# Kernel optimization log

Measured on AMD Instinct MI355X. Metric: run time of the kernel, lower is better.

The kernel has to match this reference:

```python
import jax, jax.numpy as jnp
import numpy as np

N, Q, CC = 8, 300, 92          # batch, queries, logit channels (91 classes + 1 objectness)
CF, HF, WF = 2048, 42, 42      # backbone feature map
M, TOPK = 20, 5                # GT boxes per image, pseudo-unknown top-k
NUM_CLASSES = 91
L_CLS, L_IOU, L_L1 = 2.0, 2.0, 5.0
NEG = -1e11


def cxcywh_to_xyxy(bx):
    cx, cy, bw, bh = bx[..., 0], bx[..., 1], bx[..., 2], bx[..., 3]
    return jnp.stack([cx - bw / 2, cy - bh / 2, cx + bw / 2, cy + bh / 2], -1)


def setup_inputs() -> dict:
    key = jax.random.key(0)
    ks = jax.random.split(key, 6)
    h = w = 1333
    img_features = jax.random.normal(ks[0], (N, CF, HF, WF), jnp.float32)
    pred_logits = jax.random.normal(ks[1], (N, Q, CC), jnp.float32)
    pred_boxes = jax.random.uniform(ks[2], (N, Q, 4), jnp.float32, 0.05, 0.95)
    tgt_labels = jax.random.randint(ks[3], (N, M), 0, NUM_CLASSES - 1).astype(jnp.int32)
    u = jax.random.uniform(ks[4], (N, M, 4), jnp.float32)
    # GT boxes in pixel cxcywh (bbox_normalize divides by image size)
    tgt_boxes = jnp.stack([u[..., 0] * w, u[..., 1] * h,
                           u[..., 2] * 0.3 * w + 2.0, u[..., 3] * 0.3 * h + 2.0], -1)
    perm = jax.vmap(lambda k: jax.random.permutation(k, Q))(jax.random.split(ks[5], N))
    query_idx = perm[:, :M].astype(jnp.int32)          # unique matched query per target
    tgt_idx = jnp.tile(jnp.arange(M, dtype=jnp.int32), (N, 1))
    return dict(img_features=img_features, pred_logits=pred_logits, pred_boxes=pred_boxes,
                tgt_labels=tgt_labels, tgt_boxes=tgt_boxes, query_idx=query_idx,
                tgt_idx=tgt_idx, h=h, w=w)


def _loss(img_features, pred_logits, pred_boxes, tgt_boxes, tgt_labels, query_idx, tgt_idx, h, w):
    b = jnp.arange(N)[:, None]
    scale = jnp.array([w, h, w, h], jnp.float32)
    out_prob = jnp.concatenate([jax.nn.softmax(pred_logits[..., :-1], -1),
                                jax.nn.sigmoid(pred_logits[..., -1:])], -1)  # [N,Q,92]
    matched_mask = jnp.zeros((N, Q), bool).at[b, query_idx].set(True)

    # --- per-query crop-mean pooling: bilinear upsample once + summed-area table ---
    mean_feat = jnp.mean(img_features, 1)                                  # [N,HF,WF]
    up = jax.vmap(lambda f: jax.image.resize(f, (h, w), 'bilinear'))(mean_feat)  # [N,h,w]
    sat = jnp.pad(jnp.cumsum(jnp.cumsum(up, 1), 2), ((0, 0), (1, 0), (1, 0)))    # [N,h+1,w+1]
    bb = cxcywh_to_xyxy(pred_boxes) * scale                                # pixel xyxy
    x1 = jnp.clip(bb[..., 0].astype(jnp.int32), 0, w)
    y1 = jnp.clip(bb[..., 1].astype(jnp.int32), 0, h)
    x2 = jnp.clip(bb[..., 2].astype(jnp.int32), 0, w)
    y2 = jnp.clip(bb[..., 3].astype(jnp.int32), 0, h)
    cnt = jnp.maximum(y2 - y1, 0) * jnp.maximum(x2 - x1, 0)
    x2e, y2e = jnp.maximum(x2, x1), jnp.maximum(y2, y1)
    boxsum = sat[b, y2e, x2e] - sat[b, y1, x2e] - sat[b, y2e, x1] + sat[b, y1, x1]
    means = jnp.where(cnt > 0, boxsum / jnp.maximum(cnt, 1), NEG)          # empty crop -> -1e11 (nan case)
    means = jnp.where(matched_mask, NEG, means)                            # matched queries excluded
    _, topk_idx = jax.lax.top_k(means, TOPK)                               # [N,TOPK]
    topk_mask = jnp.zeros((N, Q), bool).at[b, topk_idx].set(True)

    # --- matched terms ---
    tgt_cls = tgt_labels[b, tgt_idx]                                       # [N,M]
    tgt_bb = tgt_boxes[b, tgt_idx] / scale                                 # bbox_normalize
    q_cls = out_prob[b, query_idx, :NUM_CLASSES]                           # probs; CE re-applies log_softmax (faithful)
    q_obj = out_prob[b, query_idx, -1]
    q_bb = pred_boxes[b, query_idx]
    logp = jax.nn.log_softmax(q_cls, -1)
    ce_matched = -jnp.mean(jnp.take_along_axis(logp, tgt_cls[..., None].astype(jnp.int32), -1)[..., 0], 1)
    bce_matched = -jnp.mean(jnp.maximum(jnp.log(q_obj), -100.0), 1)
    l1 = jnp.sqrt(jnp.sum((q_bb - tgt_bb) ** 2, (1, 2)))                   # torch.dist (Frobenius)
    a, t = cxcywh_to_xyxy(q_bb), cxcywh_to_xyxy(tgt_bb)
    ix1 = jnp.maximum(a[..., 0], t[..., 0]); iy1 = jnp.maximum(a[..., 1], t[..., 1])
    ix2 = jnp.minimum(a[..., 2], t[..., 2]); iy2 = jnp.minimum(a[..., 3], t[..., 3])
    inter = jnp.clip(ix2 - ix1, 0.0) * jnp.clip(iy2 - iy1, 0.0)
    area = lambda z: (z[..., 2] - z[..., 0]) * (z[..., 3] - z[..., 1])
    iou = inter / (area(a) + area(t) - inter + 1e-9)
    iou_loss = jnp.sum(1.0 - iou, 1)

    # --- pseudo-unknown terms ---
    pk_cls = out_prob[b, topk_idx, :NUM_CLASSES]
    ce_pseudo = -jnp.mean(jax.nn.log_softmax(pk_cls, -1)[..., NUM_CLASSES - 1], 1)
    pk_obj = out_prob[b, topk_idx, -1]
    bce_topk = -jnp.mean(jnp.maximum(jnp.log(pk_obj), -100.0), 1)
    rest = (~matched_mask) & (~topk_mask)                                  # setdiff(other, topk)
    neglog1m = -jnp.maximum(jnp.log1p(-out_prob[..., -1]), -100.0)
    bce_rest = jnp.sum(jnp.where(rest, neglog1m, 0.0), 1) / jnp.maximum(jnp.sum(rest, 1), 1)

    cls_loss = jnp.sum(ce_matched + ce_pseudo)
    obj_loss = jnp.sum(bce_matched + bce_rest + bce_topk)
    return (cls_loss * L_CLS + obj_loss * L_CLS
            + jnp.sum(iou_loss) * L_IOU + jnp.sum(l1) * L_L1)


def reference(img_features, pred_logits, pred_boxes, tgt_labels, tgt_boxes, query_idx, tgt_idx, h, w):
    return _loss(img_features, pred_logits, pred_boxes, tgt_boxes, tgt_labels, query_idx, tgt_idx, h, w)
```

## Files before the change

kernel.cpp:

```cpp
#include <hip/hip_runtime.h>
#include <math.h>

#define NB 8
#define QN 300
#define CCH 92
#define NCLS 91
#define CFCH 2048
#define HFD 42
#define MT 20
#define TOPK5 5
#define DIM 1333
#define DIMF 1333.0f
#define PIX (HFD*HFD)
#define PIX4 (PIX/4)
#define CHUNKS 32
#define CPC (CFCH/CHUNKS)
#define NEGV -100000000000.0f

#define PART_BLOCKS (NB*CHUNKS*2)
#define CUM_TOTAL   (2*(DIM+1)*HFD)
#define CUM_BLOCKS  ((CUM_TOTAL + 255)/256)
#define STAT_BLOCKS ((NB*QN)/4)
#define BM_BLOCKS   ((NB*QN)/4)

__device__ __forceinline__ float bilin_w(int i, int j, float s) {
    float sf = ((float)i + 0.5f) * s - 0.5f;
    if (sf <= 0.f)                return (j == 0) ? 1.f : 0.f;
    if (sf >= (float)(HFD - 1))   return (j == HFD - 1) ? 1.f : 0.f;
    int j0 = (int)sf;
    float fr = sf - (float)j0;
    if (j == j0)     return 1.f - fr;
    if (j == j0 + 1) return fr;
    return 0.f;
}

__device__ __forceinline__ float wave_sum(float v) {
    for (int off = 32; off; off >>= 1) v += __shfl_down(v, off);
    return v;
}

__global__ __launch_bounds__(256) void stage_a(
        const float4* __restrict__ img, float4* __restrict__ part,
        float* __restrict__ CX, float* __restrict__ CY,
        const float* __restrict__ logits, const float* __restrict__ boxes,
        const int* __restrict__ query_idx, const int* __restrict__ tgt_idx,
        const int* __restrict__ tgt_labels, const float* __restrict__ tgt_boxes,
        float* __restrict__ ls2a, float* __restrict__ p90a,
        float* __restrict__ ptga, float* __restrict__ nobja,
        float* __restrict__ n1ma, float* __restrict__ l1a,
        float* __restrict__ ioua, float* __restrict__ out) {
    int blk = blockIdx.x;
    if (blk == 0 && threadIdx.x == 0) out[0] = 0.f;
    if (blk < PART_BLOCKS) {
        int tile = blk & 1;
        int chunk = (blk >> 1) & (CHUNKS - 1);
        int b = blk >> 6;
        int f = tile * 256 + threadIdx.x;
        if (f >= PIX4) return;
        const float4* p = img + (size_t)(b * CFCH + chunk * CPC) * PIX4 + f;
        float x = 0.f, y = 0.f, z = 0.f, w = 0.f;
#pragma unroll 8
        for (int k = 0; k < CPC; ++k) {
            float4 v = p[(size_t)k * PIX4];
            x += v.x; y += v.y; z += v.z; w += v.w;
        }
        float4 o; o.x = x; o.y = y; o.z = z; o.w = w;
        part[(size_t)(blk >> 1) * PIX4 + f] = o;
    } else if (blk < PART_BLOCKS + CUM_BLOCKS) {
        int idx = (blk - PART_BLOCKS) * 256 + threadIdx.x;
        const int total = (DIM + 1) * HFD;
        int t = idx / total;
        if (t >= 2) return;
        int rem = idx - t * total;
        int X = rem / HFD;
        int j = rem - X * HFD;
        const float s = (float)HFD / DIMF;
        int i0 = max(0, (int)floorf(((float)j - 0.5f) / s - 0.5f) - 2);
        int i1 = min(DIM, (int)ceilf(((float)j + 1.5f) / s - 0.5f) + 2);
        int hi = min(X, i1);
        float acc = 0.f;
        for (int i = i0; i < hi; ++i) acc += bilin_w(i, j, s);
        float* C = t ? CY : CX;
        C[X * HFD + j] = acc;
    } else {
        int gw = (blk - PART_BLOCKS - CUM_BLOCKS) * 4 + (threadIdx.x >> 6);
        int lane = threadIdx.x & 63;
        int b = gw / QN, q = gw - b * QN;
        int mpos = -1;
#pragma unroll
        for (int m = 0; m < MT; ++m) if (query_idx[b * MT + m] == q) mpos = m;
        const float* L = logits + (size_t)gw * CCH;
        float c0 = L[lane];
        float e1 = (lane < CCH - 64) ? L[lane + 64] : 0.f;
        bool has_c1 = (lane < NCLS - 64);
        float mx = fmaxf(c0, has_c1 ? e1 : -3.4e38f);
        for (int off = 32; off; off >>= 1) mx = fmaxf(mx, __shfl_xor(mx, off));
        float se = expf(c0 - mx) + (has_c1 ? expf(e1 - mx) : 0.f);
        for (int off = 32; off; off >>= 1) se += __shfl_xor(se, off);
        float inv = 1.f / se;
        float s2 = expf(expf(c0 - mx) * inv) + (has_c1 ? expf(expf(e1 - mx) * inv) : 0.f);
        for (int off = 32; off; off >>= 1) s2 += __shfl_xor(s2, off);
        float ls2 = logf(s2);
        float l90  = __shfl(e1, 26);
        float lobj = __shfl(e1, 27);
        float p90 = expf(l90 - mx) * inv;
        float sg = 1.f / (1.f + expf(-lobj));
        float nobj = -fmaxf(logf(sg), -100.f);
        float n1m  = -fmaxf(log1pf(-sg), -100.f);

        float ptg = 0.f, l1 = 0.f, iouc = 0.f;
        if (mpos >= 0) {
            const float* bx = boxes + (size_t)gw * 4;
            float cx = bx[0], cy = bx[1], bw = bx[2], bh = bx[3];
            int ti = tgt_idx[b * MT + mpos];
            int tc = tgt_labels[b * MT + ti];
            ptg = expf(L[tc] - mx) * inv;
            const float* tb = tgt_boxes + (size_t)(b * MT + ti) * 4;
            float t0 = tb[0] / DIMF, t1 = tb[1] / DIMF, t2 = tb[2] / DIMF, t3 = tb[3] / DIMF;
            float d0 = cx - t0, d1 = cy - t1, d2 = bw - t2, d3 = bh - t3;
            l1 = d0 * d0 + d1 * d1 + d2 * d2 + d3 * d3;
            float ax1 = cx - bw * 0.5f, ay1 = cy - bh * 0.5f;
            float ax2 = cx + bw * 0.5f, ay2 = cy + bh * 0.5f;
            float tx1 = t0 - t2 * 0.5f, ty1 = t1 - t3 * 0.5f;
            float tx2 = t0 + t2 * 0.5f, ty2 = t1 + t3 * 0.5f;
            float ix1 = fmaxf(ax1, tx1), iy1 = fmaxf(ay1, ty1);
            float ix2 = fminf(ax2, tx2), iy2 = fminf(ay2, ty2);
            float inter = fmaxf(ix2 - ix1, 0.f) * fmaxf(iy2 - iy1, 0.f);
            float aa = (ax2 - ax1) * (ay2 - ay1), at = (tx2 - tx1) * (ty2 - ty1);
            float iou = inter / (aa + at - inter + 1e-9f);
            iouc = 1.f - iou;
        }
        if (lane == 0) {
            ls2a[gw] = ls2; p90a[gw] = p90; ptga[gw] = ptg;
            nobja[gw] = nobj; n1ma[gw] = n1m; l1a[gw] = l1; ioua[gw] = iouc;
        }
    }
}

__global__ __launch_bounds__(256) void chan_reduce(const float* __restrict__ part,
                                                   float* __restrict__ mf) {
    int idx = blockIdx.x * 256 + threadIdx.x;
    if (idx >= NB * PIX) return;
    int b = idx / PIX, pix = idx - b * PIX;
    const float* pp = part + (size_t)b * CHUNKS * PIX + pix;
    float acc = 0.f;
#pragma unroll 8
    for (int c = 0; c < CHUNKS; ++c) acc += pp[(size_t)c * PIX];
    mf[idx] = acc * (1.0f / (float)CFCH);
}

__global__ __launch_bounds__(256) void box_means(
        const float* __restrict__ mf, const float* __restrict__ boxes,
        const int* __restrict__ query_idx,
        const float* __restrict__ CX, const float* __restrict__ CY,
        float* __restrict__ means) {
    int tid = threadIdx.x;
    int gw = (blockIdx.x * 256 + tid) >> 6;
    int lane = tid & 63, wid = tid >> 6;
    int b = gw / QN, q = gw - b * QN;

    __shared__ float s_mf[PIX];
    __shared__ float s_d[4][84];
    for (int i = tid; i < PIX; i += 256) s_mf[i] = mf[b * PIX + i];
    __syncthreads();

    int mpos = -1;
#pragma unroll
    for (int m = 0; m < MT; ++m) if (query_idx[b * MT + m] == q) mpos = m;

    const float* bx = boxes + (size_t)gw * 4;
    float cx = bx[0], cy = bx[1], bw = bx[2], bh = bx[3];
    int x1 = min(max((int)((cx - bw * 0.5f) * DIMF), 0), DIM);
    int y1 = min(max((int)((cy - bh * 0.5f) * DIMF), 0), DIM);
    int x2 = min(max((int)((cx + bw * 0.5f) * DIMF), 0), DIM);
    int y2 = min(max((int)((cy + bh * 0.5f) * DIMF), 0), DIM);
    int x2e = max(x2, x1), y2e = max(y2, y1);
    int cnt = max(y2 - y1, 0) * max(x2 - x1, 0);

    float val = NEGV;
    if (mpos < 0 && cnt > 0) {
        if (lane < HFD) {
            s_d[wid][lane]      = CY[y2e * HFD + lane] - CY[y1 * HFD + lane];
            s_d[wid][42 + lane] = CX[x2e * HFD + lane] - CX[x1 * HFD + lane];
        }
        float acc = 0.f;
#pragma unroll
        for (int i = 0; i < 28; ++i) {
            int pix = lane + (i << 6);
            if (pix < PIX) {
                int row = pix / HFD;
                int col = pix - row * HFD;
                acc += s_d[wid][row] * s_d[wid][42 + col] * s_mf[pix];
            }
        }
        acc = wave_sum(acc);
        val = acc / (float)cnt;
    }
    if (lane == 0) means[gw] = val;
}

__global__ __launch_bounds__(256) void finalize(
        const int* __restrict__ query_idx,
        const float* __restrict__ means, const float* __restrict__ ls2a,
        const float* __restrict__ p90a, const float* __restrict__ ptga,
        const float* __restrict__ nobja, const float* __restrict__ n1ma,
        const float* __restrict__ l1a, const float* __restrict__ ioua,
        float* __restrict__ out) {
    int b = blockIdx.x, tid = threadIdx.x;
    int wid = tid >> 6, lane = tid & 63;
    __shared__ float s_means[QN];
    __shared__ unsigned char s_matched[QN], s_sel[QN];
    __shared__ float s_red[4];
    __shared__ int s_redi[4];
    __shared__ float s_acc[4][8];

    for (int q = tid; q < QN; q += 256) {
        s_means[q] = means[b * QN + q];
        s_matched[q] = 0; s_sel[q] = 0;
    }
    __syncthreads();
    if (tid < MT) s_matched[query_idx[b * MT + tid]] = 1;
    __syncthreads();

    for (int r = 0; r < TOPK5; ++r) {
        float bv = -3.4e38f; int bi = QN;
        for (int q = tid; q < QN; q += 256) {
            if (!s_sel[q]) {
                float v = s_means[q];
                if (v > bv || (v == bv && q < bi)) { bv = v; bi = q; }
            }
        }
        for (int off = 32; off; off >>= 1) {
            float ov = __shfl_down(bv, off); int oi = __shfl_down(bi, off);
            if (ov > bv || (ov == bv && oi < bi)) { bv = ov; bi = oi; }
        }
        if (lane == 0) { s_red[wid] = bv; s_redi[wid] = bi; }
        __syncthreads();
        if (tid == 0) {
            float fv = s_red[0]; int fi = s_redi[0];
            for (int k = 1; k < 4; ++k)
                if (s_red[k] > fv || (s_red[k] == fv && s_redi[k] < fi)) { fv = s_red[k]; fi = s_redi[k]; }
            s_sel[fi] = 1;
        }
        __syncthreads();
    }

    float a0 = 0, a1 = 0, a2 = 0, a3 = 0, a4 = 0, a5 = 0, a6 = 0; int rc = 0;
    for (int q = tid; q < QN; q += 256) {
        int g = b * QN + q;
        if (s_matched[q]) {
            a0 += ls2a[g] - ptga[g];
            a1 += nobja[g];
            a2 += l1a[g];
            a3 += ioua[g];
        } else if (s_sel[q]) {
            a4 += ls2a[g] - p90a[g];
            a5 += nobja[g];
        } else {
            a6 += n1ma[g]; rc++;
        }
    }
    a0 = wave_sum(a0); a1 = wave_sum(a1); a2 = wave_sum(a2); a3 = wave_sum(a3);
    a4 = wave_sum(a4); a5 = wave_sum(a5); a6 = wave_sum(a6);
    float rcf = wave_sum((float)rc);
    if (lane == 0) {
        s_acc[wid][0] = a0; s_acc[wid][1] = a1; s_acc[wid][2] = a2; s_acc[wid][3] = a3;
        s_acc[wid][4] = a4; s_acc[wid][5] = a5; s_acc[wid][6] = a6; s_acc[wid][7] = rcf;
    }
    __syncthreads();
    if (tid == 0) {
        float A[8];
        for (int k = 0; k < 8; ++k)
            A[k] = s_acc[0][k] + s_acc[1][k] + s_acc[2][k] + s_acc[3][k];
        float ce_matched = A[0] / (float)MT;
        float bce_matched = A[1] / (float)MT;
        float l1 = sqrtf(A[2]);
        float iou_loss = A[3];
        float ce_pseudo = A[4] / (float)TOPK5;
        float bce_topk = A[5] / (float)TOPK5;
        int rcT = (int)(A[7] + 0.5f);
        float bce_rest = A[6] / (float)max(rcT, 1);
        float total = 2.f * (ce_matched + ce_pseudo)
                    + 2.f * (bce_matched + bce_rest + bce_topk)
                    + 2.f * iou_loss + 5.f * l1;
        atomicAdd(out, total);
    }
}

extern "C" void kernel_launch(void* const* d_in, const int* in_sizes, int n_in,
                              void* d_out, int out_size, void* d_ws, size_t ws_size,
                              hipStream_t stream) {
    const float* img        = (const float*)d_in[0];
    const float* logits     = (const float*)d_in[1];
    const float* boxes      = (const float*)d_in[2];
    const int*   tgt_labels = (const int*)d_in[3];
    const float* tgt_boxes  = (const float*)d_in[4];
    const int*   query_idx  = (const int*)d_in[5];
    const int*   tgt_idx    = (const int*)d_in[6];

    float* ws    = (float*)d_ws;
    float* part  = ws;
    float* mf    = part + (size_t)NB * CHUNKS * PIX;
    float* CX    = mf + (size_t)NB * PIX;
    float* CY    = CX + (size_t)(DIM + 1) * HFD;
    float* means = CY + (size_t)(DIM + 1) * HFD;
    float* ls2a  = means + NB * QN;
    float* p90a  = ls2a + NB * QN;
    float* ptga  = p90a + NB * QN;
    float* nobja = ptga + NB * QN;
    float* n1ma  = nobja + NB * QN;
    float* l1a   = n1ma + NB * QN;
    float* ioua  = l1a + NB * QN;

    stage_a<<<PART_BLOCKS + CUM_BLOCKS + STAT_BLOCKS, 256, 0, stream>>>(
        (const float4*)img, (float4*)part, CX, CY, logits, boxes,
        query_idx, tgt_idx, tgt_labels, tgt_boxes,
        ls2a, p90a, ptga, nobja, n1ma, l1a, ioua, (float*)d_out);
    chan_reduce<<<(NB * PIX + 255) / 256, 256, 0, stream>>>(part, mf);
    box_means<<<BM_BLOCKS, 256, 0, stream>>>(mf, boxes, query_idx, CX, CY, means);
    finalize<<<NB, 256, 0, stream>>>(query_idx, means, ls2a, p90a, ptga,
                                     nobja, n1ma, l1a, ioua, (float*)d_out);
}
```

Baseline: 202.0 us.

## Fuse channel reduce, box means and finalize into one per-image kernel

Replaces the chan_reduce, box_means and finalize kernels with a single kernel that runs one 1024-thread block per image. The channel partials are reduced into shared memory, per-query crop means are computed by 16 waves using precomputed per-lane pixel coordinates and values in registers, and top-k selection and the loss reduction follow in the same block. This removes two launches and the global round trips for the mean feature map and the query means. In exchange, the box-mean work now runs on only 8 blocks instead of hundreds.

```diff
diff --git a/kernel.cpp b/kernel.cpp
--- a/kernel.cpp
+++ b/kernel.cpp
@@ -21,7 +21,6 @@
 #define CUM_TOTAL   (2*(DIM+1)*HFD)
 #define CUM_BLOCKS  ((CUM_TOTAL + 255)/256)
 #define STAT_BLOCKS ((NB*QN)/4)
-#define BM_BLOCKS   ((NB*QN)/4)
 
 __device__ __forceinline__ float bilin_w(int i, int j, float s) {
     float sf = ((float)i + 0.5f) * s - 0.5f;
@@ -137,98 +136,79 @@
     }
 }
 
-__global__ __launch_bounds__(256) void chan_reduce(const float* __restrict__ part,
-                                                   float* __restrict__ mf) {
-    int idx = blockIdx.x * 256 + threadIdx.x;
-    if (idx >= NB * PIX) return;
-    int b = idx / PIX, pix = idx - b * PIX;
-    const float* pp = part + (size_t)b * CHUNKS * PIX + pix;
-    float acc = 0.f;
-#pragma unroll 8
-    for (int c = 0; c < CHUNKS; ++c) acc += pp[(size_t)c * PIX];
-    mf[idx] = acc * (1.0f / (float)CFCH);
-}
-
-__global__ __launch_bounds__(256) void box_means(
-        const float* __restrict__ mf, const float* __restrict__ boxes,
+__global__ __launch_bounds__(1024) void fuse_b(
+        const float* __restrict__ part, const float* __restrict__ boxes,
         const int* __restrict__ query_idx,
         const float* __restrict__ CX, const float* __restrict__ CY,
-        float* __restrict__ means) {
-    int tid = threadIdx.x;
-    int gw = (blockIdx.x * 256 + tid) >> 6;
-    int lane = tid & 63, wid = tid >> 6;
-    int b = gw / QN, q = gw - b * QN;
-
+        const float* __restrict__ ls2a, const float* __restrict__ p90a,
+        const float* __restrict__ ptga, const float* __restrict__ nobja,
+        const float* __restrict__ n1ma, const float* __restrict__ l1a,
+        const float* __restrict__ ioua, float* __restrict__ out) {
+    int b = blockIdx.x, tid = threadIdx.x;
+    int wid = tid >> 6, lane = tid & 63;
     __shared__ float s_mf[PIX];
-    __shared__ float s_d[4][84];
-    for (int i = tid; i < PIX; i += 256) s_mf[i] = mf[b * PIX + i];
-    __syncthreads();
-
-    int mpos = -1;
-#pragma unroll
-    for (int m = 0; m < MT; ++m) if (query_idx[b * MT + m] == q) mpos = m;
-
-    const float* bx = boxes + (size_t)gw * 4;
-    float cx = bx[0], cy = bx[1], bw = bx[2], bh = bx[3];
-    int x1 = min(max((int)((cx - bw * 0.5f) * DIMF), 0), DIM);
-    int y1 = min(max((int)((cy - bh * 0.5f) * DIMF), 0), DIM);
-    int x2 = min(max((int)((cx + bw * 0.5f) * DIMF), 0), DIM);
-    int y2 = min(max((int)((cy + bh * 0.5f) * DIMF), 0), DIM);
-    int x2e = max(x2, x1), y2e = max(y2, y1);
-    int cnt = max(y2 - y1, 0) * max(x2 - x1, 0);
-
-    float val = NEGV;
-    if (mpos < 0 && cnt > 0) {
-        if (lane < HFD) {
-            s_d[wid][lane]      = CY[y2e * HFD + lane] - CY[y1 * HFD + lane];
-            s_d[wid][42 + lane] = CX[x2e * HFD + lane] - CX[x1 * HFD + lane];
-        }
+    __shared__ float s_d[16][84];
+    __shared__ float s_means[QN];
+    __shared__ unsigned char s_matched[QN], s_sel[QN];
+    __shared__ float s_red[16];
+    __shared__ int   s_redi[16];
+    __shared__ float s_acc[16][8];
+
+    const float* pp = part + (size_t)b * CHUNKS * PIX;
+    for (int pix = tid; pix < PIX; pix += 1024) {
         float acc = 0.f;
 #pragma unroll
-        for (int i = 0; i < 28; ++i) {
-            int pix = lane + (i << 6);
-            if (pix < PIX) {
-                int row = pix / HFD;
-                int col = pix - row * HFD;
-                acc += s_d[wid][row] * s_d[wid][42 + col] * s_mf[pix];
-            }
-        }
-        acc = wave_sum(acc);
-        val = acc / (float)cnt;
-    }
-    if (lane == 0) means[gw] = val;
-}
-
-__global__ __launch_bounds__(256) void finalize(
-        const int* __restrict__ query_idx,
-        const float* __restrict__ means, const float* __restrict__ ls2a,
-        const float* __restrict__ p90a, const float* __restrict__ ptga,
-        const float* __restrict__ nobja, const float* __restrict__ n1ma,
-        const float* __restrict__ l1a, const float* __restrict__ ioua,
-        float* __restrict__ out) {
-    int b = blockIdx.x, tid = threadIdx.x;
-    int wid = tid >> 6, lane = tid & 63;
-    __shared__ float s_means[QN];
-    __shared__ unsigned char s_matched[QN], s_sel[QN];
-    __shared__ float s_red[4];
-    __shared__ int s_redi[4];
-    __shared__ float s_acc[4][8];
-
-    for (int q = tid; q < QN; q += 256) {
-        s_means[q] = means[b * QN + q];
-        s_matched[q] = 0; s_sel[q] = 0;
-    }
+        for (int c = 0; c < CHUNKS; ++c) acc += pp[c * PIX + pix];
+        s_mf[pix] = acc * (1.0f / (float)CFCH);
+    }
+    for (int q = tid; q < QN; q += 1024) { s_matched[q] = 0; s_sel[q] = 0; }
     __syncthreads();
     if (tid < MT) s_matched[query_idx[b * MT + tid]] = 1;
     __syncthreads();
 
+    float r_mf[28]; int r_rc[28];
+#pragma unroll
+    for (int i = 0; i < 28; ++i) {
+        int pix = lane + (i << 6);
+        if (pix < PIX) {
+            int row = pix / HFD, col = pix - row * HFD;
+            r_rc[i] = (row << 7) | col;
+            r_mf[i] = s_mf[pix];
+        } else { r_rc[i] = 0; r_mf[i] = 0.f; }
+    }
+
+    for (int q = wid; q < QN; q += 16) {
+        const float* bx = boxes + (size_t)(b * QN + q) * 4;
+        float cx = bx[0], cy = bx[1], bw = bx[2], bh = bx[3];
+        int x1 = min(max((int)((cx - bw * 0.5f) * DIMF), 0), DIM);
+        int y1 = min(max((int)((cy - bh * 0.5f) * DIMF), 0), DIM);
+        int x2 = min(max((int)((cx + bw * 0.5f) * DIMF), 0), DIM);
+        int y2 = min(max((int)((cy + bh * 0.5f) * DIMF), 0), DIM);
+        int x2e = max(x2, x1), y2e = max(y2, y1);
+        int cnt = max(y2 - y1, 0) * max(x2 - x1, 0);
+        float val = NEGV;
+        if (!s_matched[q] && cnt > 0) {
+            if (lane < HFD) {
+                s_d[wid][lane]      = CY[y2e * HFD + lane] - CY[y1 * HFD + lane];
+                s_d[wid][42 + lane] = CX[x2e * HFD + lane] - CX[x1 * HFD + lane];
+            }
+            float acc = 0.f;
+#pragma unroll
+            for (int i = 0; i < 28; ++i) {
+                int rc = r_rc[i];
+                acc += s_d[wid][rc >> 7] * s_d[wid][42 + (rc & 127)] * r_mf[i];
+            }
+            acc = wave_sum(acc);
+            val = acc / (float)cnt;
+        }
+        if (lane == 0) s_means[q] = val;
+    }
+    __syncthreads();
+
     for (int r = 0; r < TOPK5; ++r) {
         float bv = -3.4e38f; int bi = QN;
-        for (int q = tid; q < QN; q += 256) {
-            if (!s_sel[q]) {
-                float v = s_means[q];
-                if (v > bv || (v == bv && q < bi)) { bv = v; bi = q; }
-            }
+        if (tid < QN && !s_sel[tid]) {
+            bv = s_means[tid]; bi = tid;
         }
         for (int off = 32; off; off >>= 1) {
             float ov = __shfl_down(bv, off); int oi = __shfl_down(bi, off);
@@ -238,7 +218,7 @@
         __syncthreads();
         if (tid == 0) {
             float fv = s_red[0]; int fi = s_redi[0];
-            for (int k = 1; k < 4; ++k)
+            for (int k = 1; k < 16; ++k)
                 if (s_red[k] > fv || (s_red[k] == fv && s_redi[k] < fi)) { fv = s_red[k]; fi = s_redi[k]; }
             s_sel[fi] = 1;
         }
@@ -246,14 +226,14 @@
     }
 
     float a0 = 0, a1 = 0, a2 = 0, a3 = 0, a4 = 0, a5 = 0, a6 = 0; int rc = 0;
-    for (int q = tid; q < QN; q += 256) {
-        int g = b * QN + q;
-        if (s_matched[q]) {
+    if (tid < QN) {
+        int g = b * QN + tid;
+        if (s_matched[tid]) {
             a0 += ls2a[g] - ptga[g];
             a1 += nobja[g];
             a2 += l1a[g];
             a3 += ioua[g];
-        } else if (s_sel[q]) {
+        } else if (s_sel[tid]) {
             a4 += ls2a[g] - p90a[g];
             a5 += nobja[g];
         } else {
@@ -270,8 +250,11 @@
     __syncthreads();
     if (tid == 0) {
         float A[8];
-        for (int k = 0; k < 8; ++k)
-            A[k] = s_acc[0][k] + s_acc[1][k] + s_acc[2][k] + s_acc[3][k];
+        for (int k = 0; k < 8; ++k) {
+            float t = 0.f;
+            for (int w = 0; w < 16; ++w) t += s_acc[w][k];
+            A[k] = t;
+        }
         float ce_matched = A[0] / (float)MT;
         float bce_matched = A[1] / (float)MT;
         float l1 = sqrtf(A[2]);
@@ -300,11 +283,9 @@
 
     float* ws    = (float*)d_ws;
     float* part  = ws;
-    float* mf    = part + (size_t)NB * CHUNKS * PIX;
-    float* CX    = mf + (size_t)NB * PIX;
+    float* CX    = part + (size_t)NB * CHUNKS * PIX;
     float* CY    = CX + (size_t)(DIM + 1) * HFD;
-    float* means = CY + (size_t)(DIM + 1) * HFD;
-    float* ls2a  = means + NB * QN;
+    float* ls2a  = CY + (size_t)(DIM + 1) * HFD;
     float* p90a  = ls2a + NB * QN;
     float* ptga  = p90a + NB * QN;
     float* nobja = ptga + NB * QN;
@@ -316,8 +297,7 @@
         (const float4*)img, (float4*)part, CX, CY, logits, boxes,
         query_idx, tgt_idx, tgt_labels, tgt_boxes,
         ls2a, p90a, ptga, nobja, n1ma, l1a, ioua, (float*)d_out);
-    chan_reduce<<<(NB * PIX + 255) / 256, 256, 0, stream>>>(part, mf);
-    box_means<<<BM_BLOCKS, 256, 0, stream>>>(mf, boxes, query_idx, CX, CY, means);
-    finalize<<<NB, 256, 0, stream>>>(query_idx, means, ls2a, p90a, ptga,
-                                     nobja, n1ma, l1a, ioua, (float*)d_out);
-}
+    fuse_b<<<NB, 1024, 0, stream>>>(part, boxes, query_idx, CX, CY,
+                                    ls2a, p90a, ptga, nobja, n1ma, l1a, ioua,
+                                    (float*)d_out);
+}
```

Result: slower. 227.7 us (+12.7%).
